# Performance work log

Measured on AMD Instinct MI355X. Metric: run time of the kernel, lower is better.

## Reference

```python
import jax, jax.numpy as jnp
import numpy as np

B, S, D = 8, 2048, 1024
H = 4 * D  # MLP hidden


def setup_inputs() -> dict:
    key = jax.random.key(0)
    ks = jax.random.split(key, 10)
    scale = 0.02
    return {
        "x": jax.random.normal(ks[0], (B, S, D), dtype=jnp.float32),
        "ln_gamma": jnp.ones((D,), jnp.float32),
        "ln_beta": jnp.zeros((D,), jnp.float32),
        "Wq": jax.random.normal(ks[1], (D, D), jnp.float32) * scale,
        "Wk": jax.random.normal(ks[2], (D, D), jnp.float32) * scale,
        "Wv": jax.random.normal(ks[3], (D, D), jnp.float32) * scale,
        "W1": jax.random.normal(ks[4], (D, H), jnp.float32) * scale,
        "b1": jnp.zeros((H,), jnp.float32),
        "W2": jax.random.normal(ks[5], (H, D), jnp.float32) * scale,
        "b2": jnp.zeros((D,), jnp.float32),
    }


def _forward(x, ln_gamma, ln_beta, Wq, Wk, Wv, W1, b1, W2, b2):
    shortcut = x
    # LayerNorm (eps=1e-5, torch default)
    mu = jnp.mean(x, axis=-1, keepdims=True)
    var = jnp.mean((x - mu) ** 2, axis=-1, keepdims=True)
    xn = (x - mu) * jax.lax.rsqrt(var + 1e-5) * ln_gamma + ln_beta
    # Self-attention (note: scale applied AFTER softmax, as in source)
    q = jnp.einsum("bsd,de->bse", xn, Wq)
    k = jnp.einsum("bsd,de->bse", xn, Wk)
    v = jnp.einsum("bsd,de->bse", xn, Wv)
    scores = jnp.einsum("bqe,bke->bqk", q, k)  # [B,S,S]
    atten = jax.nn.softmax(scores, axis=-1) * (1.0 / np.sqrt(D))
    out = jnp.einsum("bqk,bke->bqe", atten, v)
    # dropout is identity at inference
    # MLP: Linear -> Swish -> Linear
    h = jnp.einsum("bsd,dh->bsh", out, W1) + b1
    h = h * jax.nn.sigmoid(h)
    y = jnp.einsum("bsh,hd->bsd", h, W2) + b2
    return y + shortcut


def reference(x, ln_gamma, ln_beta, Wq, Wk, Wv, W1, b1, W2, b2):
    return _forward(x, ln_gamma, ln_beta, Wq, Wk, Wv, W1, b1, W2, b2)
```

## Files before the change

kernel.cpp:

```cpp
#include <hip/hip_runtime.h>
#include <hip/hip_fp8.h>


#define Bb_ 8
#define Ss_ 2048
#define Dd_ 1024
#define Hh_ 4096

typedef __bf16 bf16;
typedef _Float16 f16;
typedef unsigned char u8;
typedef unsigned int u32;
typedef unsigned long long u64;
typedef __attribute__((ext_vector_type(8))) _Float16 f16x8;
typedef __attribute__((ext_vector_type(4))) float f32x4;

enum { EPI_QKV = 0, EPI_SCORE = 1, EPI_AOS = 2, EPI_SWISH = 3, EPI_RESID = 4 };

__device__ __forceinline__ void gload16(const void* g, void* l) {
  __builtin_amdgcn_global_load_lds(
      (const __attribute__((address_space(1))) void*)g,
      (__attribute__((address_space(3))) void*)l, 16, 0, 0);
}

__device__ __forceinline__ u8 to_fp8(float f) {
  __hip_fp8_e4m3 v(f);
  return (u8)v.__x;
}

#define SETP(x) __builtin_amdgcn_s_setprio(x)
#define BARRIER()                          \
  do {                                     \
    asm volatile("" ::: "memory");         \
    __builtin_amdgcn_s_barrier();          \
    asm volatile("" ::: "memory");         \
  } while (0)
#define VMC(n) asm volatile("s_waitcnt vmcnt(" #n ")" ::: "memory")

__global__ __launch_bounds__(256) void tcast8_k(const float* __restrict__ W,
                                                u8* __restrict__ WT, int K, int N) {
  __shared__ float tile[32][33];
  const int tn0 = blockIdx.x * 32;
  const int tk0 = blockIdx.y * 32;
  const int t = threadIdx.x;
  const int c = t & 31;
  const int r4 = t >> 5;
#pragma unroll
  for (int i = 0; i < 4; i++) {
    int r = r4 + i * 8;
    tile[r][c] = W[(long)(tk0 + r) * N + (tn0 + c)];
  }
  __syncthreads();
#pragma unroll
  for (int i = 0; i < 4; i++) {
    int r = r4 + i * 8;
    WT[(long)(tn0 + r) * K + (tk0 + c)] = to_fp8(tile[c][r]);
  }
}

__global__ __launch_bounds__(256) void tv8_k(const f16* __restrict__ V,
                                             u8* __restrict__ VT) {
  __shared__ f16 tile[64][72];
  const long z = blockIdx.z;
  const int n0 = blockIdx.x * 64;
  const int k0 = blockIdx.y * 64;
  const int t = threadIdx.x;
  const int r = t >> 3;
  const int c = (t & 7) * 8;
  const f16* Vb = V + z * (long)(Ss_ * Dd_);
  u8* VTb = VT + z * (long)(Dd_ * Ss_);
#pragma unroll
  for (int i = 0; i < 2; i++)
    *(f16x8*)&tile[r + i * 32][c] =
        *(const f16x8*)(Vb + (long)(k0 + r + i * 32) * Dd_ + n0 + c);
  __syncthreads();
#pragma unroll
  for (int i = 0; i < 2; i++) {
    const int n = r + i * 32;
    union { u8 b[8]; u64 w; } ov;
#pragma unroll
    for (int j = 0; j < 8; j++) ov.b[j] = to_fp8((float)tile[c + j][n]);
    *(u64*)(VTb + (long)(n0 + n) * Ss_ + k0 + c) = ov.w;
  }
}

__global__ __launch_bounds__(256) void ln8_k(const float* __restrict__ x,
                                             const float* __restrict__ gamma,
                                             const float* __restrict__ beta,
                                             u8* __restrict__ xn) {
  const long row = blockIdx.x;
  const float* xr = x + row * Dd_;
  const int t = threadIdx.x;
  float4 v = *(const float4*)(xr + t * 4);
  float s = v.x + v.y + v.z + v.w;
  float sq = v.x * v.x + v.y * v.y + v.z * v.z + v.w * v.w;
#pragma unroll
  for (int o = 32; o > 0; o >>= 1) {
    s += __shfl_down(s, o);
    sq += __shfl_down(sq, o);
  }
  __shared__ float ls[4], lq[4];
  const int wid = t >> 6;
  if ((t & 63) == 0) { ls[wid] = s; lq[wid] = sq; }
  __syncthreads();
  if (t == 0) {
    float S = ls[0] + ls[1] + ls[2] + ls[3];
    float Q = lq[0] + lq[1] + lq[2] + lq[3];
    float mu = S * (1.0f / Dd_);
    float var = Q * (1.0f / Dd_) - mu * mu;
    ls[0] = mu;
    lq[0] = rsqrtf(var + 1e-5f);
  }
  __syncthreads();
  const float mu = ls[0], rstd = lq[0];
  float4 g = *(const float4*)(gamma + t * 4);
  float4 be = *(const float4*)(beta + t * 4);
  u32 pk = (u32)to_fp8((v.x - mu) * rstd * g.x + be.x) |
           ((u32)to_fp8((v.y - mu) * rstd * g.y + be.y) << 8) |
           ((u32)to_fp8((v.z - mu) * rstd * g.z + be.z) << 16) |
           ((u32)to_fp8((v.w - mu) * rstd * g.w + be.w) << 24);
  *(u32*)(xn + row * (long)Dd_ + t * 4) = pk;
}

__global__ __launch_bounds__(256) void softmax8_k(f16* __restrict__ lo,
                                                  f16* __restrict__ hi) {
  const long row = blockIdx.x;
  const long z = row >> 11;
  f16* sr = (z < 4 ? lo + z * 4194304L : hi + (z - 4) * 4194304L) +
            (row & 2047) * (long)Ss_;
  const int t = threadIdx.x;
  f16x8 v = *(const f16x8*)(sr + t * 8);
  float f[8];
#pragma unroll
  for (int j = 0; j < 8; j++) f[j] = (float)v[j];
  float vm = f[0];
#pragma unroll
  for (int j = 1; j < 8; j++) vm = fmaxf(vm, f[j]);
  __shared__ float red[4];
#pragma unroll
  for (int o = 32; o > 0; o >>= 1) vm = fmaxf(vm, __shfl_xor(vm, o));
  const int wid = t >> 6;
  if ((t & 63) == 0) red[wid] = vm;
  __syncthreads();
  vm = fmaxf(fmaxf(red[0], red[1]), fmaxf(red[2], red[3]));
  float e[8], s = 0.f;
#pragma unroll
  for (int j = 0; j < 8; j++) { e[j] = __expf(f[j] - vm); s += e[j]; }
#pragma unroll
  for (int o = 32; o > 0; o >>= 1) s += __shfl_xor(s, o);
  __syncthreads();
  if ((t & 63) == 0) red[wid] = s;
  __syncthreads();
  s = red[0] + red[1] + red[2] + red[3];
  const float rs = 256.0f / s;
  union { u8 b[8]; u64 w; } ov;
#pragma unroll
  for (int j = 0; j < 8; j++) ov.b[j] = to_fp8(e[j] * rs);
  *(u64*)((u8*)sr + t * 8) = ov.w;
}

template <int EPI>
__global__ __launch_bounds__(256, 2) void gemmq_k(
    const u8* __restrict__ Ab, const u8* __restrict__ Bbp, void* __restrict__ Cb,
    const float* __restrict__ bias, const float* __restrict__ resid,
    int K, int lda, int ldb, int ldc, long astr, long bstr, long cstr) {
  extern __shared__ u8 Lq[];
  const int t = threadIdx.x;
  const int lane = t & 63;
  const int w = t >> 6;
  const int wm = w >> 1, wn = w & 1;

  const int gx = gridDim.x;
  const int nwg = gx * gridDim.y;
  const int dd = blockIdx.y * gx + blockIdx.x;
  const int cpx = nwg >> 3;
  const int xcd = dd & 7;
  const int idx = dd >> 3;
  const int R = cpx / gx;
  const int H = (R >= 8) ? 8 : R;
  const int bandsz = H * gx;
  const int bnd = idx / bandsz;
  const int rr = idx % bandsz;
  const int m_t = xcd * R + bnd * H + (rr % H);
  const int n_t = rr / H;
  const int m0 = m_t * 128;
  const int n0 = n_t * 128;

  const long z = blockIdx.z;
  const u8* A;
  if constexpr (EPI == EPI_RESID) {
    const long qo[4] = {0, 67108864, 100663296, 134217728};
    A = Ab + qo[m0 >> 12] - (long)(m0 & ~4095) * lda;
  } else if constexpr (EPI == EPI_AOS) {
    A = (z < 4) ? Ab + z * astr : (const u8*)bias + (z - 4) * astr;
  } else if constexpr (EPI == EPI_SWISH) {
    A = Ab;
  } else {
    A = Ab + z * astr;
  }
  const u8* Bp = Bbp + z * bstr;

  const int lrow = lane >> 3;
  const int sc = 16 * ((lane & 7) ^ ((lane >> 3) & 7));
  const u8* gA[4];
  const u8* gB[4];
#pragma unroll
  for (int j = 0; j < 4; ++j) {
    const int r = (w * 4 + j) * 8 + lrow;
    gA[j] = A + (long)(m0 + r) * lda + sc;
    gB[j] = Bp + (long)(n0 + r) * ldb + sc;
  }

#define QSTAGE(buf, tau)                                                         \
  do {                                                                           \
    _Pragma("unroll") for (int j_ = 0; j_ < 4; ++j_)                             \
        gload16(gA[j_] + (long)(tau) * 128,                                      \
                &Lq[(buf)*32768 + (w * 4 + j_) * 1024]);                         \
    _Pragma("unroll") for (int j_ = 0; j_ < 4; ++j_)                             \
        gload16(gB[j_] + (long)(tau) * 128,                                      \
                &Lq[(buf)*32768 + 16384 + (w * 4 + j_) * 1024]);                 \
  } while (0)

  const int rA = lane & 15;
  const int kq = lane >> 4;

#define QREAD_ALL(base)                                                          \
  _Pragma("unroll") for (int q_ = 0; q_ < 4; ++q_)                               \
  _Pragma("unroll") for (int ks_ = 0; ks_ < 4; ++ks_) {                          \
    const int ra_ = wm * 64 + q_ * 16 + rA;                                      \
    const int rb_ = wn * 64 + q_ * 16 + rA;                                      \
    const int kb_ = ks_ * 32 + kq * 8;                                           \
    a[q_][ks_] = *(const u64*)&Lq[(base) + ra_ * 128 +                           \
                                  (((kb_ >> 4) ^ (ra_ & 7)) << 4) + (kb_ & 8)];  \
    b[q_][ks_] = *(const u64*)&Lq[(base) + 16384 + rb_ * 128 +                   \
                                  (((kb_ >> 4) ^ (rb_ & 7)) << 4) + (kb_ & 8)];  \
  }
#define QMFMA_ALL()                                                              \
  do {                                                                           \
    SETP(1);                                                                     \
    _Pragma("unroll") for (int ks = 0; ks < 4; ++ks)                             \
    _Pragma("unroll") for (int q = 0; q < 4; ++q)                                \
    _Pragma("unroll") for (int p = 0; p < 4; ++p)                                \
        acc[q][p] = __builtin_amdgcn_mfma_f32_16x16x32_fp8_fp8(                  \
            (long)a[q][ks], (long)b[p][ks], acc[q][p], 0, 0, 0);                 \
    SETP(0);                                                                     \
  } while (0)

  f32x4 acc[4][4] = {};
  u64 a[4][4], b[4][4];

  QSTAGE(0, 0);
  QSTAGE(1, 1);

  const int NT = K >> 7;
  for (int tt = 0; tt < NT; tt += 2) {
    VMC(8);
    BARRIER();
    QREAD_ALL(0);
    QMFMA_ALL();
    BARRIER();
    if (tt + 2 < NT) QSTAGE(0, tt + 2);
    if (tt + 2 < NT) VMC(8); else VMC(0);
    BARRIER();
    QREAD_ALL(32768);
    QMFMA_ALL();
    BARRIER();
    if (tt + 3 < NT) QSTAGE(1, tt + 3);
  }

  const int row0 = m0 + wm * 64;
  const int col0 = n0 + wn * 64;
  const int cl = lane & 15;
  const int rg = (lane >> 4) * 4;
#pragma unroll
  for (int mi = 0; mi < 4; mi++) {
#pragma unroll
    for (int ni = 0; ni < 4; ni++) {
#pragma unroll
      for (int j = 0; j < 4; j++) {
        const long gm = row0 + mi * 16 + rg + j;
        const int gn = col0 + ni * 16 + cl;
        float val = acc[mi][ni][j];
        if constexpr (EPI == EPI_QKV) {
          if (z < 2) {
            ((u8*)Cb)[z * cstr + gm * ldc + gn] = to_fp8(val);
          } else {
            ((f16*)resid)[gm * (long)ldc + gn] = (f16)val;
          }
        } else if constexpr (EPI == EPI_SCORE) {
          f16* dst = (z < 4) ? (f16*)Cb : (f16*)bias;
          dst[(z & 3) * cstr + gm * ldc + gn] = (f16)val;
        } else if constexpr (EPI == EPI_AOS) {
          ((u8*)Cb)[z * cstr + gm * ldc + gn] = to_fp8(val * (1.0f / 8192.0f));
        } else if constexpr (EPI == EPI_SWISH) {
          const long qoc[4] = {0, 67108864, 100663296, 134217728};
          u8* hq = (u8*)Cb + qoc[m0 >> 12];
          float hv = val + bias[gn];
          hq[(long)(gm & 4095) * ldc + gn] = to_fp8(hv / (1.0f + __expf(-hv)));
        } else {
          ((float*)Cb)[gm * (long)ldc + gn] = val + bias[gn] + resid[gm * (long)ldc + gn];
        }
      }
    }
  }
#undef QSTAGE
#undef QREAD_ALL
#undef QMFMA_ALL
}

extern "C" void kernel_launch(void* const* d_in, const int* in_sizes, int n_in,
                              void* d_out, int out_size, void* d_ws, size_t ws_size,
                              hipStream_t stream) {
  const float* x  = (const float*)d_in[0];
  const float* g  = (const float*)d_in[1];
  const float* be = (const float*)d_in[2];
  const float* Wq = (const float*)d_in[3];
  const float* Wk = (const float*)d_in[4];
  const float* Wv = (const float*)d_in[5];
  const float* W1 = (const float*)d_in[6];
  const float* b1 = (const float*)d_in[7];
  const float* W2 = (const float*)d_in[8];
  const float* b2 = (const float*)d_in[9];

  hipFuncSetAttribute((const void*)&gemmq_k<EPI_QKV>,
                      hipFuncAttributeMaxDynamicSharedMemorySize, 65536);
  hipFuncSetAttribute((const void*)&gemmq_k<EPI_SCORE>,
                      hipFuncAttributeMaxDynamicSharedMemorySize, 65536);
  hipFuncSetAttribute((const void*)&gemmq_k<EPI_AOS>,
                      hipFuncAttributeMaxDynamicSharedMemorySize, 65536);
  hipFuncSetAttribute((const void*)&gemmq_k<EPI_SWISH>,
                      hipFuncAttributeMaxDynamicSharedMemorySize, 65536);
  hipFuncSetAttribute((const void*)&gemmq_k<EPI_RESID>,
                      hipFuncAttributeMaxDynamicSharedMemorySize, 65536);

  char* ws = (char*)d_ws;
  u8*   xn8       = (u8*)(ws + 0);
  f16*  scores_lo = (f16*)(ws + 0);
  u8*   q8        = (u8*)(ws + 33554432);
  u8*   ao8       = (u8*)(ws + 33554432);
  u8*   k8        = (u8*)(ws + 50331648);
  f16*  vrows     = (f16*)(ws + 67108864);
  f16*  scores_hi = (f16*)(ws + 100663296);
  u8*   vT8       = (u8*)(ws + 134217728);
  u8*   wq8       = (u8*)(ws + 167772160);
  u8*   w1T8      = (u8*)(ws + 170917888);
  u8*   w2T8      = (u8*)(ws + 175112192);

  tcast8_k<<<dim3(32, 32), 256, 0, stream>>>(Wq, wq8, 1024, 1024);
  tcast8_k<<<dim3(32, 32), 256, 0, stream>>>(Wk, wq8 + 1048576, 1024, 1024);
  tcast8_k<<<dim3(32, 32), 256, 0, stream>>>(Wv, wq8 + 2097152, 1024, 1024);
  tcast8_k<<<dim3(128, 32), 256, 0, stream>>>(W1, w1T8, 1024, 4096);
  tcast8_k<<<dim3(32, 128), 256, 0, stream>>>(W2, w2T8, 4096, 1024);

  ln8_k<<<16384, 256, 0, stream>>>(x, g, be, xn8);

  gemmq_k<EPI_QKV><<<dim3(8, 128, 3), 256, 65536, stream>>>(
      xn8, wq8, q8, nullptr, (const float*)vrows,
      1024, 1024, 1024, 1024, 0L, 1048576L, 16777216L);

  tv8_k<<<dim3(16, 32, 8), 256, 0, stream>>>(vrows, vT8);

  gemmq_k<EPI_SCORE><<<dim3(16, 16, 8), 256, 65536, stream>>>(
      q8, k8, scores_lo, (const float*)scores_hi, nullptr,
      1024, 1024, 1024, 2048, 2097152L, 2097152L, 4194304L);

  softmax8_k<<<16384, 256, 0, stream>>>(scores_lo, scores_hi);

  gemmq_k<EPI_AOS><<<dim3(8, 16, 8), 256, 65536, stream>>>(
      (const u8*)scores_lo, vT8, ao8, (const float*)scores_hi, nullptr,
      2048, 4096, 2048, 1024, 8388608L, 2097152L, 2097152L);

  gemmq_k<EPI_SWISH><<<dim3(32, 128, 1), 256, 65536, stream>>>(
      ao8, w1T8, ws, b1, nullptr, 1024, 1024, 1024, 4096, 0L, 0L, 0L);
  gemmq_k<EPI_RESID><<<dim3(8, 128, 1), 256, 65536, stream>>>(
      (const u8*)ws, w2T8, d_out, b2, x, 4096, 4096, 4096, 1024, 0L, 0L, 0L);
}
```

Baseline: 486.8 us.

## Use 16x16x128 scaled FP8 MFMA and fuse QKV projections into one grid

Replaces the 16x16x32 fp8 MFMA (four k-steps per 128-wide tile) with the gfx950 mfma_scale 16x16x128 f8f6f4 instruction using unit scales. LDS reads become two 16-byte vector loads per row instead of four 8-byte loads. The QKV GEMM is launched as a single 24x128 grid over the concatenated weight, with outputs routed by n0. The aim is fewer MFMA issues, fewer LDS instructions and a single larger launch. It relies on the swizzled layout and register fragment order matching the new instruction's operand layout.

```diff
diff --git a/kernel.cpp b/kernel.cpp
--- a/kernel.cpp
+++ b/kernel.cpp
@@ -14,6 +14,8 @@
 typedef unsigned long long u64;
 typedef __attribute__((ext_vector_type(8))) _Float16 f16x8;
 typedef __attribute__((ext_vector_type(4))) float f32x4;
+typedef __attribute__((ext_vector_type(4))) int i32x4;
+typedef __attribute__((ext_vector_type(8))) int i32x8;
 
 enum { EPI_QKV = 0, EPI_SCORE = 1, EPI_AOS = 2, EPI_SWISH = 3, EPI_RESID = 4 };
 
@@ -193,7 +195,7 @@
     A = Ab + qo[m0 >> 12] - (long)(m0 & ~4095) * lda;
   } else if constexpr (EPI == EPI_AOS) {
     A = (z < 4) ? Ab + z * astr : (const u8*)bias + (z - 4) * astr;
-  } else if constexpr (EPI == EPI_SWISH) {
+  } else if constexpr (EPI == EPI_SWISH || EPI == EPI_QKV) {
     A = Ab;
   } else {
     A = Ab + z * astr;
@@ -222,32 +224,37 @@
   } while (0)
 
   const int rA = lane & 15;
-  const int kq = lane >> 4;
+  const int g2 = (lane >> 4) * 2;
 
 #define QREAD_ALL(base)                                                          \
-  _Pragma("unroll") for (int q_ = 0; q_ < 4; ++q_)                               \
-  _Pragma("unroll") for (int ks_ = 0; ks_ < 4; ++ks_) {                          \
+  _Pragma("unroll") for (int q_ = 0; q_ < 4; ++q_) {                             \
     const int ra_ = wm * 64 + q_ * 16 + rA;                                      \
     const int rb_ = wn * 64 + q_ * 16 + rA;                                      \
-    const int kb_ = ks_ * 32 + kq * 8;                                           \
-    a[q_][ks_] = *(const u64*)&Lq[(base) + ra_ * 128 +                           \
-                                  (((kb_ >> 4) ^ (ra_ & 7)) << 4) + (kb_ & 8)];  \
-    b[q_][ks_] = *(const u64*)&Lq[(base) + 16384 + rb_ * 128 +                   \
-                                  (((kb_ >> 4) ^ (rb_ & 7)) << 4) + (kb_ & 8)];  \
+    i32x4 alo = *(const i32x4*)&Lq[(base) + ra_ * 128 +                          \
+                                   ((g2 ^ (ra_ & 7)) << 4)];                     \
+    i32x4 ahi = *(const i32x4*)&Lq[(base) + ra_ * 128 +                          \
+                                   (((g2 + 1) ^ (ra_ & 7)) << 4)];               \
+    i32x4 blo = *(const i32x4*)&Lq[(base) + 16384 + rb_ * 128 +                  \
+                                   ((g2 ^ (rb_ & 7)) << 4)];                     \
+    i32x4 bhi = *(const i32x4*)&Lq[(base) + 16384 + rb_ * 128 +                  \
+                                   (((g2 + 1) ^ (rb_ & 7)) << 4)];               \
+    _Pragma("unroll") for (int j_ = 0; j_ < 4; ++j_) {                           \
+      av[q_][j_] = alo[j_]; av[q_][4 + j_] = ahi[j_];                            \
+      bv[q_][j_] = blo[j_]; bv[q_][4 + j_] = bhi[j_];                            \
+    }                                                                            \
   }
 #define QMFMA_ALL()                                                              \
   do {                                                                           \
     SETP(1);                                                                     \
-    _Pragma("unroll") for (int ks = 0; ks < 4; ++ks)                             \
     _Pragma("unroll") for (int q = 0; q < 4; ++q)                                \
     _Pragma("unroll") for (int p = 0; p < 4; ++p)                                \
-        acc[q][p] = __builtin_amdgcn_mfma_f32_16x16x32_fp8_fp8(                  \
-            (long)a[q][ks], (long)b[p][ks], acc[q][p], 0, 0, 0);                 \
+        acc[q][p] = __builtin_amdgcn_mfma_scale_f32_16x16x128_f8f6f4(            \
+            av[q], bv[p], acc[q][p], 0, 0, 0, 0x7F, 0, 0x7F);                    \
     SETP(0);                                                                     \
   } while (0)
 
   f32x4 acc[4][4] = {};
-  u64 a[4][4], b[4][4];
+  i32x8 av[4], bv[4];
 
   QSTAGE(0, 0);
   QSTAGE(1, 1);
@@ -282,10 +289,12 @@
         const int gn = col0 + ni * 16 + cl;
         float val = acc[mi][ni][j];
         if constexpr (EPI == EPI_QKV) {
-          if (z < 2) {
-            ((u8*)Cb)[z * cstr + gm * ldc + gn] = to_fp8(val);
+          if (n0 < 1024) {
+            ((u8*)Cb)[gm * (long)ldc + gn] = to_fp8(val);
+          } else if (n0 < 2048) {
+            ((u8*)Cb)[16777216L + gm * (long)ldc + (gn & 1023)] = to_fp8(val);
           } else {
-            ((f16*)resid)[gm * (long)ldc + gn] = (f16)val;
+            ((f16*)resid)[gm * (long)ldc + (gn & 1023)] = (f16)val;
           }
         } else if constexpr (EPI == EPI_SCORE) {
           f16* dst = (z < 4) ? (f16*)Cb : (f16*)bias;
@@ -354,9 +363,9 @@
 
   ln8_k<<<16384, 256, 0, stream>>>(x, g, be, xn8);
 
-  gemmq_k<EPI_QKV><<<dim3(8, 128, 3), 256, 65536, stream>>>(
+  gemmq_k<EPI_QKV><<<dim3(24, 128, 1), 256, 65536, stream>>>(
       xn8, wq8, q8, nullptr, (const float*)vrows,
-      1024, 1024, 1024, 1024, 0L, 1048576L, 16777216L);
+      1024, 1024, 1024, 1024, 0L, 0L, 0L);
 
   tv8_k<<<dim3(16, 32, 8), 256, 0, stream>>>(vrows, vT8);
 
```

New measurement: 401.8 us. 1.21x faster.
